# Performance work log

Hardware: AMD Instinct MI355X
Metric: run time of the kernel (lower is better)

The kernel has to match this reference:

```python
import jax, jax.numpy as jnp
import numpy as np


def mha_col0(x0, w_in, b_in, w_out, b_out):
    # x0: [N, D]. torch MHA (1 head, batch_first=False): seq dim = N, this is the
    # batch-0 slice (the only one consumed by tmp[:, 0]).
    qkv = x0 @ w_in.T + b_in                     # [N, 3D]
    q, k, v = jnp.split(qkv, 3, axis=-1)         # each [N, D]
    scale = 1.0 / np.sqrt(np.float32(q.shape[-1]))
    attn = jax.nn.softmax((q * scale) @ k.T, axis=-1)   # [N, N]
    return (attn @ v) @ w_out.T + b_out          # [N, D]


def sage(x_src, x_dst, ei, w_l, b_l, w_r):
    # PyG SAGEConv with aggr='sum': out = lin_l(sum_j x_src[src_j]) + lin_r(x_dst)
    msg = x_src[ei[0]]                                            # [E, D] gather
    agg = jax.ops.segment_sum(msg, ei[1], num_segments=x_dst.shape[0])  # [Nd, D] scatter
    return agg @ w_l.T + b_l + x_dst @ w_r.T


def setup_inputs() -> dict:
    key = jax.random.key(0)
    ks = jax.random.split(key, 24)
    N, C, D, E = 8192, 6, 128, 262144
    s = 0.05
    p = lambda k, shape: jax.random.normal(k, shape, dtype=jnp.float32) * s
    return {
        "x_A": jax.random.normal(ks[0], (N, C, D), dtype=jnp.float32),
        "x_B": jax.random.normal(ks[1], (N, C, D), dtype=jnp.float32),
        "ei_AB": jax.random.randint(ks[2], (2, E), 0, N),
        "ei_BA": jax.random.randint(ks[3], (2, E), 0, N),
        "ei_AA": jax.random.randint(ks[4], (2, E), 0, N),
        "inW_A": p(ks[5], (3 * D, D)), "inB_A": p(ks[6], (3 * D,)),
        "outW_A": p(ks[7], (D, D)), "outB_A": p(ks[8], (D,)),
        "inW_B": p(ks[9], (3 * D, D)), "inB_B": p(ks[10], (3 * D,)),
        "outW_B": p(ks[11], (D, D)), "outB_B": p(ks[12], (D,)),
        "wl_AB": p(ks[13], (D, D)), "bl_AB": p(ks[14], (D,)), "wr_AB": p(ks[15], (D, D)),
        "wl_BA": p(ks[16], (D, D)), "bl_BA": p(ks[17], (D,)), "wr_BA": p(ks[18], (D, D)),
        "wl_AA": p(ks[19], (D, D)), "bl_AA": p(ks[20], (D,)), "wr_AA": p(ks[21], (D, D)),
    }


def reference(x_A, x_B, ei_AB, ei_BA, ei_AA,
              inW_A, inB_A, outW_A, outB_A,
              inW_B, inB_B, outW_B, outB_B,
              wl_AB, bl_AB, wr_AB,
              wl_BA, bl_BA, wr_BA,
              wl_AA, bl_AA, wr_AA):
    # per-type attention, keeping only column 0 (tmp[:, 0])
    h_A = mha_col0(x_A[:, 0], inW_A, inB_A, outW_A, outB_A)   # [N, D]
    h_B = mha_col0(x_B[:, 0], inW_B, inB_B, outW_B, outB_B)   # [N, D]
    # HeteroConv(aggr='sum'): B gets A->B; A gets B->A + A->A
    out_B = sage(h_A, h_B, ei_AB, wl_AB, bl_AB, wr_AB)
    out_A = (sage(h_B, h_A, ei_BA, wl_BA, bl_BA, wr_BA)
             + sage(h_A, h_A, ei_AA, wl_AA, bl_AA, wr_AA))
    # re-attach remaining column tokens (x is 3D)
    new_A = jnp.concatenate((out_A[:, None, :], x_A[:, 1:]), axis=1)  # [N, C, D]
    new_B = jnp.concatenate((out_B[:, None, :], x_B[:, 1:]), axis=1)
    return new_A, new_B
```

## Files before the change

### kernel.cpp

```cpp
#include <hip/hip_runtime.h>
#include <hip/hip_bf16.h>

typedef unsigned short u16;
typedef unsigned int u32;
typedef __attribute__((ext_vector_type(8))) short bf16x8;
typedef __attribute__((ext_vector_type(4))) short bf16x4;
typedef __attribute__((ext_vector_type(4))) float f32x4;
typedef __attribute__((ext_vector_type(16))) float f32x16;

#define MFMA(a,b,c)   __builtin_amdgcn_mfma_f32_16x16x32_bf16((a),(b),(c),0,0,0)
#define MFMA32(a,b,c) __builtin_amdgcn_mfma_f32_32x32x16_bf16((a),(b),(c),0,0,0)

__device__ __forceinline__ float bf2f(u16 u){
  union { float f; u32 i; } c; c.i = ((u32)u) << 16; return c.f;
}
__device__ __forceinline__ u16 f2bf(float f){
  __hip_bfloat16 h = __float2bfloat16(f);
  u16 u; __builtin_memcpy(&u, &h, 2); return u;
}
__device__ __forceinline__ bf16x8 ld8f(const float* p){
  bf16x8 r;
  #pragma unroll
  for (int i = 0; i < 8; i++) r[i] = (short)f2bf(p[i]);
  return r;
}
__device__ __forceinline__ u32 cvtpk(float a, float b){
  u32 r; asm volatile("v_cvt_pk_bf16_f32 %0, %1, %2" : "=v"(r) : "v"(a), "v"(b)); return r;
}
__device__ __forceinline__ void pl32swap(u32 &a, u32 &b){
  asm volatile("v_permlane32_swap_b32 %0, %1" : "+v"(a), "+v"(b));
}

#define QSCALE 0.12751741528681559f

struct WPrepArgs { const float* src[10]; int off[10]; int total4; };
__global__ __launch_bounds__(256) void prelude_kernel(
    WPrepArgs a, u16* __restrict__ wdst,
    const int* __restrict__ e0, const int* __restrict__ e1, const int* __restrict__ e2,
    int* __restrict__ cnt,
    const float* __restrict__ xA, float* __restrict__ outA,
    const float* __restrict__ xB, float* __restrict__ outB,
    int Nn, int E, int W, int HB, int TB)
{
  const int tid = threadIdx.x;
  int b = blockIdx.x;
  if (b < W) {
    int i = b * 256 + tid;
    if (i >= a.total4) return;
    int e = i * 4;
    int j = 0;
    #pragma unroll
    for (int k = 1; k < 10; k++) if (e >= a.off[k]) j = k;
    f32x4 v = *(const f32x4*)(a.src[j] + (e - a.off[j]));
    bf16x4 o;
    #pragma unroll
    for (int r = 0; r < 4; r++) o[r] = (short)f2bf(v[r]);
    *(bf16x4*)(wdst + e) = o;
    return;
  }
  b -= W;
  if (b < 3 * HB) {
    int t = b / HB;
    int e = (b % HB) * 256 + tid;
    if (e >= E) return;
    const int* ei = t == 0 ? e0 : (t == 1 ? e1 : e2);
    atomicAdd(&cnt[t * Nn + ei[E + e]], 1);
    return;
  }
  b -= 3 * HB;
  {
    int t = b / TB;
    int idx = (b % TB) * 256 + tid;
    if (idx >= Nn * 160) return;
    const float* x = t ? xB : xA;
    float* o = t ? outB : outA;
    int n = idx / 160, r = idx % 160;
    size_t off = (size_t)n * 768 + 128 + (size_t)r * 4;
    *(f32x4*)(o + off) = *(const f32x4*)(x + off);
  }
}

__global__ __launch_bounds__(256) void qkv_scan_kernel(
    const float* __restrict__ xA, const u16* __restrict__ wA, const float* __restrict__ bA, u16* __restrict__ yA,
    const float* __restrict__ xB, const u16* __restrict__ wB, const float* __restrict__ bB, u16* __restrict__ yB,
    u16* __restrict__ vtA_, u16* __restrict__ vtB_,
    const int* __restrict__ cnt, int* __restrict__ off, int* __restrict__ work,
    int Nn, int N, int LB)
{
  const int tid = threadIdx.x;
  int b = blockIdx.x;
  if (b >= 2 * LB) {
    const int t = b - 2 * LB;
    const int* c = cnt + t * Nn;
    int* o = off + t * (Nn + 1);
    int* w = work + t * Nn;
    __shared__ int part[256];
    const int base = tid * 32;
    int loc[32], s = 0;
    #pragma unroll
    for (int i = 0; i < 32; i++) { loc[i] = s; s += c[base + i]; }
    part[tid] = s;
    __syncthreads();
    #pragma unroll
    for (int st = 1; st < 256; st <<= 1) {
      int v = (tid >= st) ? part[tid - st] : 0;
      __syncthreads();
      part[tid] += v;
      __syncthreads();
    }
    int pre = (tid == 0) ? 0 : part[tid - 1];
    #pragma unroll
    for (int i = 0; i < 32; i++) { int p = pre + loc[i]; o[base + i] = p; w[base + i] = p; }
    if (tid == 255) o[Nn] = part[255];
    return;
  }
  const int yb = b & 1, xb = b >> 1;
  const float* x = yb ? xB : xA;
  const u16* w = yb ? wB : wA;
  const float* bb = yb ? bB : bA;
  u16* y = yb ? yB : yA;
  u16* vt = yb ? vtB_ : vtA_;
  const int lane = tid & 63, wid = tid >> 6;
  const int g = lane >> 4, l15 = lane & 15;
  const int row0 = xb * 64 + wid * 16;

  bf16x8 a[4];
  const float* xr = x + (size_t)(row0 + l15) * 768;
  #pragma unroll
  for (int kk = 0; kk < 4; kk++) a[kk] = ld8f(xr + kk * 32 + g * 8);

  const f32x4 fz = {0.f, 0.f, 0.f, 0.f};
  for (int j0 = 0; j0 < 384; j0 += 16) {
    f32x4 acc = fz;
    const u16* wr_ = w + (size_t)(j0 + l15) * 128;
    #pragma unroll
    for (int kk = 0; kk < 4; kk++)
      acc = MFMA(a[kk], *(const bf16x8*)(wr_ + kk * 32 + g * 8), acc);
    float bv = bb[j0 + l15];
    if (j0 < 128) {
      #pragma unroll
      for (int r = 0; r < 4; r++)
        y[(size_t)(row0 + g * 4 + r) * 256 + j0 + l15] = f2bf((acc[r] + bv) * QSCALE);
    } else if (j0 < 256) {
      #pragma unroll
      for (int r = 0; r < 4; r++)
        y[(size_t)(row0 + g * 4 + r) * 256 + j0 + l15] = f2bf(acc[r] + bv);
    } else {
      bf16x4 o4;
      #pragma unroll
      for (int r = 0; r < 4; r++) o4[r] = (short)f2bf(acc[r] + bv);
      *(bf16x4*)(vt + (size_t)(j0 - 256 + l15) * N + row0 + g * 4) = o4;
    }
  }
}

__global__ __launch_bounds__(256, 2) void flash_sort_kernel(
    const u16* __restrict__ qkvA, const u16* __restrict__ vtA,
    const u16* __restrict__ qkvB, const u16* __restrict__ vtB,
    u16* __restrict__ part_acc, float* __restrict__ part_ml,
    const int* __restrict__ e0, const int* __restrict__ e1, const int* __restrict__ e2,
    int* __restrict__ work, int* __restrict__ ssrc,
    int N, int segsz, int SEG, int NB128, int FB, int HB, int E)
{
  __shared__ __align__(16) u16 Kt[2][64 * 128];
  __shared__ __align__(16) u16 Vtt[3][128 * 64];
  const int tid = threadIdx.x;
  int b = blockIdx.x;
  if (b >= FB) {
    int sb = b - FB;
    int t = sb / HB;
    int e = (sb % HB) * 256 + tid;
    if (e >= E) return;
    const int* ei = t == 0 ? e0 : (t == 1 ? e1 : e2);
    int s = ei[e], d = ei[E + e];
    int pos = atomicAdd(&work[t * N + d], 1);
    ssrc[(size_t)t * E + pos] = s;
    return;
  }
  const int x = b % NB128;
  const int rest = b / NB128;
  const int seg = rest % SEG;
  const int ty = rest / SEG;
  const u16* qkv = ty ? qkvB : qkvA;
  const u16* vt  = ty ? vtB  : vtA;
  const int lane = tid & 63, wid = tid >> 6;
  const int l31 = lane & 31, h = lane >> 5, l7 = lane & 7;
  const int q = x * 128 + wid * 32 + l31;
  const int kvbase = seg * segsz;
  const int nt = segsz >> 6;

  int rk[4], ck[4], cks[4], rv[4], cv[4], cvs[4];
  #pragma unroll
  for (int i = 0; i < 4; i++) {
    int ch = tid + i * 256;
    rk[i] = ch >> 4; ck[i] = (ch & 15) * 8; cks[i] = ck[i] ^ ((rk[i] & 7) << 3);
    rv[i] = ch >> 3; cv[i] = (ch & 7) * 8;  cvs[i] = cv[i] ^ ((rv[i] & 7) << 3);
  }

  bf16x8 aQ[8];
  const u16* qr = qkv + (size_t)q * 256;
  #pragma unroll
  for (int kk = 0; kk < 8; kk++) aQ[kk] = *(const bf16x8*)(qr + kk * 16 + h * 8);

  f32x16 accO[4];
  #pragma unroll
  for (int d = 0; d < 4; d++) accO[d] = (f32x16)0.f;
  float m_ = -INFINITY, l_ = 0.f;
  f32x16 scA[2], scB[2];
  bf16x8 kreg[4], vreg[4];

  #pragma unroll
  for (int i = 0; i < 4; i++) {
    kreg[i] = *(const bf16x8*)(qkv + 128 + (size_t)(kvbase + rk[i]) * 256 + ck[i]);
    vreg[i] = *(const bf16x8*)(vt + (size_t)rv[i] * N + kvbase + cv[i]);
  }
  #pragma unroll
  for (int i = 0; i < 4; i++) {
    *(bf16x8*)&Kt[0][rk[i] * 128 + cks[i]] = kreg[i];
    *(bf16x8*)&Vtt[0][rv[i] * 64 + cvs[i]] = vreg[i];
  }
  __syncthreads();
  if (nt > 1) {
    const int kv1 = kvbase + 64;
    #pragma unroll
    for (int i = 0; i < 4; i++) {
      kreg[i] = *(const bf16x8*)(qkv + 128 + (size_t)(kv1 + rk[i]) * 256 + ck[i]);
      vreg[i] = *(const bf16x8*)(vt + (size_t)rv[i] * N + kv1 + cv[i]);
    }
  }
  scA[0] = (f32x16)0.f; scA[1] = (f32x16)0.f;
  #pragma unroll
  for (int kk = 0; kk < 8; kk++) {
    const int co = ((kk * 2 + h) * 8) ^ (l7 << 3);
    bf16x8 aK0 = *(bf16x8*)&Kt[0][l31 * 128 + co];
    bf16x8 aK1 = *(bf16x8*)&Kt[0][(32 + l31) * 128 + co];
    scA[0] = MFMA32(aK0, aQ[kk], scA[0]);
    scA[1] = MFMA32(aK1, aQ[kk], scA[1]);
  }

  int t = 0, vb = 0;
  auto fstep = [&](f32x16* scIn, f32x16* scOut) {
    const bool hasN = (t + 1 < nt);
    const int kbN = (t + 1) & 1;
    const int vbN = (vb + 1 == 3) ? 0 : vb + 1;
    if (hasN) {
      #pragma unroll
      for (int i = 0; i < 4; i++) {
        *(bf16x8*)&Kt[kbN][rk[i] * 128 + cks[i]] = kreg[i];
        *(bf16x8*)&Vtt[vbN][rv[i] * 64 + cvs[i]] = vreg[i];
      }
    }
    __syncthreads();
    if (t + 2 < nt) {
      const int kv0n = kvbase + (t + 2) * 64;
      #pragma unroll
      for (int i = 0; i < 4; i++) {
        kreg[i] = *(const bf16x8*)(qkv + 128 + (size_t)(kv0n + rk[i]) * 256 + ck[i]);
        vreg[i] = *(const bf16x8*)(vt + (size_t)rv[i] * N + kv0n + cv[i]);
      }
    }
    if (hasN) {
      scOut[0] = (f32x16)0.f; scOut[1] = (f32x16)0.f;
      #pragma unroll
      for (int kk = 0; kk < 8; kk++) {
        const int co = ((kk * 2 + h) * 8) ^ (l7 << 3);
        bf16x8 aK0 = *(bf16x8*)&Kt[kbN][l31 * 128 + co];
        bf16x8 aK1 = *(bf16x8*)&Kt[kbN][(32 + l31) * 128 + co];
        scOut[0] = MFMA32(aK0, aQ[kk], scOut[0]);
        scOut[1] = MFMA32(aK1, aQ[kk], scOut[1]);
      }
    }
    float pmax = scIn[0][0];
    #pragma unroll
    for (int i = 1; i < 16; i++) pmax = fmaxf(pmax, scIn[0][i]);
    #pragma unroll
    for (int i = 0; i < 16; i++) pmax = fmaxf(pmax, scIn[1][i]);
    pmax = fmaxf(pmax, __shfl_xor(pmax, 32));
    if (!__all(pmax - m_ <= 8.0f)) {
      float nm = fmaxf(m_, pmax);
      float corr = __builtin_exp2f(m_ - nm);
      m_ = nm; l_ *= corr;
      #pragma unroll
      for (int d = 0; d < 4; d++)
        #pragma unroll
        for (int i = 0; i < 16; i++) accO[d][i] *= corr;
    }
    float sum = 0.f;
    #pragma unroll
    for (int i = 0; i < 16; i++) {
      float e0 = __builtin_exp2f(scIn[0][i] - m_);
      float e1 = __builtin_exp2f(scIn[1][i] - m_);
      scIn[0][i] = e0; scIn[1][i] = e1; sum += e0 + e1;
    }
    sum += __shfl_xor(sum, 32);
    l_ += sum;
    #pragma unroll
    for (int tt = 0; tt < 4; tt++) {
      const f32x16& s_ = scIn[tt >> 1];
      const int jA = (tt & 1) * 2, jB = jA + 1;
      u32 a0 = cvtpk(s_[jA * 4 + 0], s_[jA * 4 + 1]);
      u32 b0 = cvtpk(s_[jB * 4 + 0], s_[jB * 4 + 1]);
      u32 a1 = cvtpk(s_[jA * 4 + 2], s_[jA * 4 + 3]);
      u32 b1 = cvtpk(s_[jB * 4 + 2], s_[jB * 4 + 3]);
      pl32swap(a0, b0); pl32swap(a1, b1);
      union { u32 w[4]; bf16x8 v; } pf;
      pf.w[0] = a0; pf.w[1] = a1; pf.w[2] = b0; pf.w[3] = b1;
      #pragma unroll
      for (int db = 0; db < 4; db++) {
        bf16x8 aV = *(bf16x8*)&Vtt[vb][(db * 32 + l31) * 64 + (((tt * 2 + h) * 8) ^ (l7 << 3))];
        accO[db] = MFMA32(aV, pf.v, accO[db]);
      }
    }
    vb = vbN; ++t;
  };
  while (t < nt) { fstep(scA, scB); fstep(scB, scA); }

  const size_t pbase = ((size_t)(ty * SEG + seg) * N + q) * 128;
  #pragma unroll
  for (int d = 0; d < 4; d++)
    #pragma unroll
    for (int j = 0; j < 4; j++) {
      bf16x4 o4;
      #pragma unroll
      for (int r = 0; r < 4; r++) o4[r] = (short)f2bf(accO[d][j * 4 + r]);
      *(bf16x4*)(part_acc + pbase + d * 32 + j * 8 + h * 4) = o4;
    }
  if (h == 0) {
    float2 ml; ml.x = m_; ml.y = l_;
    *(float2*)(part_ml + ((size_t)(ty * SEG + seg) * N + q) * 2) = ml;
  }
}

__global__ __launch_bounds__(256) void combine_hproj_kernel(
    const u16* __restrict__ part_acc, const float* __restrict__ part_ml,
    const u16* __restrict__ woutA, const float* __restrict__ boutA, u16* __restrict__ hA,
    const u16* __restrict__ woutB, const float* __restrict__ boutB, u16* __restrict__ hB,
    int N, int SEG)
{
  __shared__ __align__(16) u16 ot[64 * 136];
  const int t = blockIdx.y;
  const u16* w = t ? woutB : woutA;
  const float* bb = t ? boutB : boutA;
  u16* hOut = t ? hB : hA;
  const int tid = threadIdx.x;
  const int row = tid >> 2, qt = tid & 3;
  const int grow = blockIdx.x * 64 + row;

  float m = -INFINITY;
  for (int s = 0; s < SEG; s++)
    m = fmaxf(m, part_ml[((size_t)(t * SEG + s) * N + grow) * 2]);
  float l = 0.f;
  float acc[32];
  #pragma unroll
  for (int i = 0; i < 32; i++) acc[i] = 0.f;
  for (int s = 0; s < SEG; s++) {
    const float* ml = part_ml + ((size_t)(t * SEG + s) * N + grow) * 2;
    float w8 = __builtin_exp2f(ml[0] - m);
    l += w8 * ml[1];
    const u16* pa = part_acc + ((size_t)(t * SEG + s) * N + grow) * 128 + qt * 32;
    #pragma unroll
    for (int j = 0; j < 4; j++) {
      bf16x8 vch = *(const bf16x8*)(pa + j * 8);
      #pragma unroll
      for (int i = 0; i < 8; i++) acc[j * 8 + i] += w8 * bf2f((u16)vch[i]);
    }
  }
  const float inv = 1.f / l;
  #pragma unroll
  for (int j = 0; j < 4; j++) {
    bf16x8 oc;
    #pragma unroll
    for (int i = 0; i < 8; i++) oc[i] = (short)f2bf(acc[j * 8 + i] * inv);
    *(bf16x8*)&ot[row * 136 + qt * 32 + j * 8] = oc;
  }
  __syncthreads();

  const int lane = tid & 63, wid = tid >> 6;
  const int g = lane >> 4, l15 = lane & 15;
  const int row0 = wid * 16;
  bf16x8 a[4];
  #pragma unroll
  for (int kk = 0; kk < 4; kk++) a[kk] = *(bf16x8*)&ot[(row0 + l15) * 136 + kk * 32 + g * 8];
  const f32x4 fz = {0.f, 0.f, 0.f, 0.f};
  for (int j0 = 0; j0 < 128; j0 += 16) {
    f32x4 acc2 = fz;
    const u16* wr_ = w + (size_t)(j0 + l15) * 128;
    #pragma unroll
    for (int kk = 0; kk < 4; kk++)
      acc2 = MFMA(a[kk], *(const bf16x8*)(wr_ + kk * 32 + g * 8), acc2);
    float bv = bb[j0 + l15];
    #pragma unroll
    for (int r = 0; r < 4; r++)
      hOut[(size_t)(blockIdx.x * 64 + row0 + g * 4 + r) * 128 + j0 + l15] = f2bf(acc2[r] + bv);
  }
}

__global__ __launch_bounds__(256) void aggregate_kernel(
    const u16* __restrict__ h0, const u16* __restrict__ h1, const u16* __restrict__ h2,
    const int* __restrict__ off, const int* __restrict__ ssrc,
    u16* __restrict__ agg, int Nn, int E)
{
  const int t = blockIdx.y;
  const u16* h = t == 0 ? h0 : (t == 1 ? h1 : h2);
  const int* o = off + t * (Nn + 1);
  const int* ss = ssrc + (size_t)t * E;
  u16* a = agg + (size_t)t * Nn * 128;
  const int wid = threadIdx.x >> 6, lane = threadIdx.x & 63;
  const int d = blockIdx.x * 4 + wid;
  const int s0 = o[d], s1 = o[d + 1];
  float a0 = 0.f, a1 = 0.f;
  int e = s0;
  for (; e + 3 < s1; e += 4) {
    int r0 = ss[e], r1 = ss[e + 1], r2 = ss[e + 2], r3 = ss[e + 3];
    u32 v0 = *(const u32*)(h + (size_t)r0 * 128 + lane * 2);
    u32 v1 = *(const u32*)(h + (size_t)r1 * 128 + lane * 2);
    u32 v2 = *(const u32*)(h + (size_t)r2 * 128 + lane * 2);
    u32 v3 = *(const u32*)(h + (size_t)r3 * 128 + lane * 2);
    a0 += bf2f((u16)(v0 & 0xffff)) + bf2f((u16)(v1 & 0xffff)) + bf2f((u16)(v2 & 0xffff)) + bf2f((u16)(v3 & 0xffff));
    a1 += bf2f((u16)(v0 >> 16)) + bf2f((u16)(v1 >> 16)) + bf2f((u16)(v2 >> 16)) + bf2f((u16)(v3 >> 16));
  }
  for (; e < s1; e++) {
    u32 v = *(const u32*)(h + (size_t)ss[e] * 128 + lane * 2);
    a0 += bf2f((u16)(v & 0xffff));
    a1 += bf2f((u16)(v >> 16));
  }
  *(u32*)(a + (size_t)d * 128 + lane * 2) = cvtpk(a0, a1);
}

__global__ __launch_bounds__(256) void sage_out_kernel(
    const u16* __restrict__ aggAB, const u16* __restrict__ wlAB, const float* __restrict__ blAB,
    const u16* __restrict__ hB, const u16* __restrict__ wrAB,
    const u16* __restrict__ aggBA, const u16* __restrict__ wlBA, const float* __restrict__ blBA,
    const u16* __restrict__ hA, const u16* __restrict__ wrBA,
    const u16* __restrict__ aggAA, const u16* __restrict__ wlAA, const float* __restrict__ blAA,
    const u16* __restrict__ wrAA,
    float* __restrict__ outA, float* __restrict__ outB)
{
  const bool two = (blockIdx.y == 1);
  const u16* agg1 = two ? aggBA : aggAB;
  const u16* wl1  = two ? wlBA  : wlAB;
  const float* bl1 = two ? blBA : blAB;
  const u16* h1   = two ? hA : hB;
  const u16* wr1  = two ? wrBA : wrAB;
  float* out = two ? outA : outB;

  const int lane = threadIdx.x & 63, wid = threadIdx.x >> 6;
  const int g = lane >> 4, l15 = lane & 15;
  const int row0 = blockIdx.x * 64 + wid * 16;

  bf16x8 a1[4], aH1[4], a2[4];
  const u16* ar1 = agg1 + (size_t)(row0 + l15) * 128;
  const u16* hr1 = h1 + (size_t)(row0 + l15) * 128;
  #pragma unroll
  for (int kk = 0; kk < 4; kk++) {
    a1[kk] = *(const bf16x8*)(ar1 + kk * 32 + g * 8);
    aH1[kk] = *(const bf16x8*)(hr1 + kk * 32 + g * 8);
  }
  if (two) {
    const u16* ar2 = aggAA + (size_t)(row0 + l15) * 128;
    #pragma unroll
    for (int kk = 0; kk < 4; kk++)
      a2[kk] = *(const bf16x8*)(ar2 + kk * 32 + g * 8);
  }

  const f32x4 fz = {0.f, 0.f, 0.f, 0.f};
  for (int j0 = 0; j0 < 128; j0 += 16) {
    f32x4 acc = fz;
    const u16* w1 = wl1 + (size_t)(j0 + l15) * 128;
    const u16* w2 = wr1 + (size_t)(j0 + l15) * 128;
    #pragma unroll
    for (int kk = 0; kk < 4; kk++) {
      acc = MFMA(a1[kk], *(const bf16x8*)(w1 + kk * 32 + g * 8), acc);
      acc = MFMA(aH1[kk], *(const bf16x8*)(w2 + kk * 32 + g * 8), acc);
    }
    float bias = bl1[j0 + l15];
    if (two) {
      const u16* w3 = wlAA + (size_t)(j0 + l15) * 128;
      const u16* w4 = wrAA + (size_t)(j0 + l15) * 128;
      #pragma unroll
      for (int kk = 0; kk < 4; kk++) {
        acc = MFMA(a2[kk], *(const bf16x8*)(w3 + kk * 32 + g * 8), acc);
        acc = MFMA(aH1[kk], *(const bf16x8*)(w4 + kk * 32 + g * 8), acc);
      }
      bias += blAA[j0 + l15];
    }
    #pragma unroll
    for (int r = 0; r < 4; r++)
      out[(size_t)(row0 + g * 4 + r) * 768 + j0 + l15] = acc[r] + bias;
  }
}

extern "C" void kernel_launch(void* const* d_in, const int* in_sizes, int n_in,
                              void* d_out, int out_size, void* d_ws, size_t ws_size,
                              hipStream_t stream)
{
  const int D = 128, C = 6;
  const int N = in_sizes[0] / (C * D);
  const int E = in_sizes[2] / 2;

  const float* xA = (const float*)d_in[0];
  const float* xB = (const float*)d_in[1];
  const int* eiAB = (const int*)d_in[2];
  const int* eiBA = (const int*)d_in[3];
  const int* eiAA = (const int*)d_in[4];
  const float* inW_A  = (const float*)d_in[5];
  const float* inB_A  = (const float*)d_in[6];
  const float* outW_A = (const float*)d_in[7];
  const float* outB_A = (const float*)d_in[8];
  const float* inW_B  = (const float*)d_in[9];
  const float* inB_B  = (const float*)d_in[10];
  const float* outW_B = (const float*)d_in[11];
  const float* outB_B = (const float*)d_in[12];
  const float* wlAB = (const float*)d_in[13];
  const float* blAB = (const float*)d_in[14];
  const float* wrAB = (const float*)d_in[15];
  const float* wlBA = (const float*)d_in[16];
  const float* blBA = (const float*)d_in[17];
  const float* wrBA = (const float*)d_in[18];
  const float* wlAA = (const float*)d_in[19];
  const float* blAA = (const float*)d_in[20];
  const float* wrAA = (const float*)d_in[21];

  u16* qkvA = (u16*)d_ws;
  u16* qkvB = qkvA + (size_t)N * 256;
  u16* vtA  = qkvB + (size_t)N * 256;
  u16* vtB  = vtA + (size_t)D * N;
  u16* hA   = vtB + (size_t)D * N;
  u16* hB   = hA + (size_t)N * D;
  u16* wbf  = hB + (size_t)N * D;
  const int wsz[10] = {3*D*D, 3*D*D, D*D, D*D, D*D, D*D, D*D, D*D, D*D, D*D};
  const float* wsrc[10] = {inW_A, inW_B, outW_A, outW_B, wlAB, wrAB, wlBA, wrBA, wlAA, wrAA};
  WPrepArgs wp; int wtot = 0;
  for (int k = 0; k < 10; k++) { wp.src[k] = wsrc[k]; wp.off[k] = wtot; wtot += wsz[k]; }
  wp.total4 = wtot / 4;
  u16* w_inA  = wbf + wp.off[0];
  u16* w_inB  = wbf + wp.off[1];
  u16* w_outA = wbf + wp.off[2];
  u16* w_outB = wbf + wp.off[3];
  u16* w_wlAB = wbf + wp.off[4];
  u16* w_wrAB = wbf + wp.off[5];
  u16* w_wlBA = wbf + wp.off[6];
  u16* w_wrBA = wbf + wp.off[7];
  u16* w_wlAA = wbf + wp.off[8];
  u16* w_wrAA = wbf + wp.off[9];

  int* cnt  = (int*)(wbf + wtot);
  int* off  = cnt + 3 * N;
  int* work = off + 3 * (N + 1);
  int* ssrc = work + 3 * N;
  char* uni = (char*)(ssrc + 3 * E);
  size_t base_b = (size_t)(uni - (char*)d_ws);
  size_t agg_b = (size_t)3 * N * 128 * 2;
  auto part_b = [&](int S){ return (size_t)2 * S * N * 128 * 2 + (size_t)2 * S * N * 2 * 4; };
  int SEG = 4;
  while (SEG > 1 && ws_size < base_b + (part_b(SEG) > agg_b ? part_b(SEG) : agg_b)) SEG >>= 1;
  const int segsz = N / SEG;
  u16* part_acc = (u16*)uni;
  float* part_ml = (float*)(part_acc + (size_t)2 * SEG * N * 128);
  u16* aggAB = (u16*)uni;
  u16* aggBA = aggAB + (size_t)N * D;
  u16* aggAA = aggBA + (size_t)N * D;

  float* outA = (float*)d_out;
  float* outB = outA + (size_t)N * C * D;

  dim3 blk(256);
  const int W = (wp.total4 + 255) / 256;
  const int HB = (E + 255) / 256;
  const int TB = (N * 160 + 255) / 256;
  const int LB = N / 64;
  const int NB128 = N / 128;
  const int FB = NB128 * SEG * 2;
  (void)hipMemsetAsync(cnt, 0, (size_t)3 * N * sizeof(int), stream);
  prelude_kernel<<<dim3(W + 3 * HB + 2 * TB), blk, 0, stream>>>(
      wp, wbf, eiAB, eiBA, eiAA, cnt, xA, outA, xB, outB, N, E, W, HB, TB);
  qkv_scan_kernel<<<dim3(2 * LB + 3), blk, 0, stream>>>(
      xA, w_inA, inB_A, qkvA, xB, w_inB, inB_B, qkvB, vtA, vtB,
      cnt, off, work, N, N, LB);
  flash_sort_kernel<<<dim3(FB + 3 * HB), blk, 0, stream>>>(
      qkvA, vtA, qkvB, vtB, part_acc, part_ml,
      eiAB, eiBA, eiAA, work, ssrc, N, segsz, SEG, NB128, FB, HB, E);
  combine_hproj_kernel<<<dim3(N / 64, 2), blk, 0, stream>>>(part_acc, part_ml,
                                                            w_outA, outB_A, hA,
                                                            w_outB, outB_B, hB, N, SEG);
  aggregate_kernel<<<dim3(N / 4, 3), blk, 0, stream>>>(hA, hB, hA, off, ssrc, aggAB, N, E);
  sage_out_kernel<<<dim3(N / 64, 2), blk, 0, stream>>>(
      aggAB, w_wlAB, blAB, hB, w_wrAB,
      aggBA, w_wlBA, blBA, hA, w_wrBA,
      aggAA, w_wlAA, blAA, w_wrAA, outA, outB);
}
```

Measured before the change: 236.1 us.

## Drop LDS staging in flash attention; read K/V directly from global memory

The flash attention kernel no longer stages K and V tiles through double/triple-buffered shared memory with barriers and register prefetch. Each wave now loads its MFMA operands for K and V straight from global memory (relying on L1/L2 caching). It also raises the launch-bounds occupancy hint to 3 blocks per CU and doubles the KV split count to 8 segments for more parallelism. The trade-off is redundant global/L2 traffic across the four waves and no explicit latency hiding, against removing LDS writes and syncs and gaining occupancy.

New measurement: 426.5 us. 1.81x slower.

```diff
diff --git a/kernel.cpp b/kernel.cpp
--- a/kernel.cpp
+++ b/kernel.cpp
@@ -154,7 +154,7 @@
   }
 }
 
-__global__ __launch_bounds__(256, 2) void flash_sort_kernel(
+__global__ __launch_bounds__(256, 3) void flash_sort_kernel(
     const u16* __restrict__ qkvA, const u16* __restrict__ vtA,
     const u16* __restrict__ qkvB, const u16* __restrict__ vtB,
     u16* __restrict__ part_acc, float* __restrict__ part_ml,
@@ -162,8 +162,6 @@
     int* __restrict__ work, int* __restrict__ ssrc,
     int N, int segsz, int SEG, int NB128, int FB, int HB, int E)
 {
-  __shared__ __align__(16) u16 Kt[2][64 * 128];
-  __shared__ __align__(16) u16 Vtt[3][128 * 64];
   const int tid = threadIdx.x;
   int b = blockIdx.x;
   if (b >= FB) {
@@ -184,18 +182,9 @@
   const u16* qkv = ty ? qkvB : qkvA;
   const u16* vt  = ty ? vtB  : vtA;
   const int lane = tid & 63, wid = tid >> 6;
-  const int l31 = lane & 31, h = lane >> 5, l7 = lane & 7;
+  const int l31 = lane & 31, h = lane >> 5;
   const int q = x * 128 + wid * 32 + l31;
   const int kvbase = seg * segsz;
-  const int nt = segsz >> 6;
-
-  int rk[4], ck[4], cks[4], rv[4], cv[4], cvs[4];
-  #pragma unroll
-  for (int i = 0; i < 4; i++) {
-    int ch = tid + i * 256;
-    rk[i] = ch >> 4; ck[i] = (ch & 15) * 8; cks[i] = ck[i] ^ ((rk[i] & 7) << 3);
-    rv[i] = ch >> 3; cv[i] = (ch & 7) * 8;  cvs[i] = cv[i] ^ ((rv[i] & 7) << 3);
-  }
 
   bf16x8 aQ[8];
   const u16* qr = qkv + (size_t)q * 256;
@@ -206,75 +195,27 @@
   #pragma unroll
   for (int d = 0; d < 4; d++) accO[d] = (f32x16)0.f;
   float m_ = -INFINITY, l_ = 0.f;
-  f32x16 scA[2], scB[2];
-  bf16x8 kreg[4], vreg[4];
-
-  #pragma unroll
-  for (int i = 0; i < 4; i++) {
-    kreg[i] = *(const bf16x8*)(qkv + 128 + (size_t)(kvbase + rk[i]) * 256 + ck[i]);
-    vreg[i] = *(const bf16x8*)(vt + (size_t)rv[i] * N + kvbase + cv[i]);
-  }
-  #pragma unroll
-  for (int i = 0; i < 4; i++) {
-    *(bf16x8*)&Kt[0][rk[i] * 128 + cks[i]] = kreg[i];
-    *(bf16x8*)&Vtt[0][rv[i] * 64 + cvs[i]] = vreg[i];
-  }
-  __syncthreads();
-  if (nt > 1) {
-    const int kv1 = kvbase + 64;
-    #pragma unroll
-    for (int i = 0; i < 4; i++) {
-      kreg[i] = *(const bf16x8*)(qkv + 128 + (size_t)(kv1 + rk[i]) * 256 + ck[i]);
-      vreg[i] = *(const bf16x8*)(vt + (size_t)rv[i] * N + kv1 + cv[i]);
-    }
-  }
-  scA[0] = (f32x16)0.f; scA[1] = (f32x16)0.f;
-  #pragma unroll
-  for (int kk = 0; kk < 8; kk++) {
-    const int co = ((kk * 2 + h) * 8) ^ (l7 << 3);
-    bf16x8 aK0 = *(bf16x8*)&Kt[0][l31 * 128 + co];
-    bf16x8 aK1 = *(bf16x8*)&Kt[0][(32 + l31) * 128 + co];
-    scA[0] = MFMA32(aK0, aQ[kk], scA[0]);
-    scA[1] = MFMA32(aK1, aQ[kk], scA[1]);
-  }
-
-  int t = 0, vb = 0;
-  auto fstep = [&](f32x16* scIn, f32x16* scOut) {
-    const bool hasN = (t + 1 < nt);
-    const int kbN = (t + 1) & 1;
-    const int vbN = (vb + 1 == 3) ? 0 : vb + 1;
-    if (hasN) {
-      #pragma unroll
-      for (int i = 0; i < 4; i++) {
-        *(bf16x8*)&Kt[kbN][rk[i] * 128 + cks[i]] = kreg[i];
-        *(bf16x8*)&Vtt[vbN][rv[i] * 64 + cvs[i]] = vreg[i];
-      }
-    }
-    __syncthreads();
-    if (t + 2 < nt) {
-      const int kv0n = kvbase + (t + 2) * 64;
-      #pragma unroll
-      for (int i = 0; i < 4; i++) {
-        kreg[i] = *(const bf16x8*)(qkv + 128 + (size_t)(kv0n + rk[i]) * 256 + ck[i]);
-        vreg[i] = *(const bf16x8*)(vt + (size_t)rv[i] * N + kv0n + cv[i]);
-      }
-    }
-    if (hasN) {
-      scOut[0] = (f32x16)0.f; scOut[1] = (f32x16)0.f;
-      #pragma unroll
-      for (int kk = 0; kk < 8; kk++) {
-        const int co = ((kk * 2 + h) * 8) ^ (l7 << 3);
-        bf16x8 aK0 = *(bf16x8*)&Kt[kbN][l31 * 128 + co];
-        bf16x8 aK1 = *(bf16x8*)&Kt[kbN][(32 + l31) * 128 + co];
-        scOut[0] = MFMA32(aK0, aQ[kk], scOut[0]);
-        scOut[1] = MFMA32(aK1, aQ[kk], scOut[1]);
-      }
-    }
-    float pmax = scIn[0][0];
-    #pragma unroll
-    for (int i = 1; i < 16; i++) pmax = fmaxf(pmax, scIn[0][i]);
-    #pragma unroll
-    for (int i = 0; i < 16; i++) pmax = fmaxf(pmax, scIn[1][i]);
+
+  const u16* kp = qkv + 128 + (size_t)l31 * 256 + h * 8;
+  const u16* vp = vt + (size_t)l31 * N + h * 8;
+
+  for (int kv0 = kvbase; kv0 < kvbase + segsz; kv0 += 64) {
+    const u16* kt0 = kp + (size_t)kv0 * 256;
+    const u16* kt1 = kt0 + 32 * 256;
+    f32x16 sc0 = (f32x16)0.f, sc1 = (f32x16)0.f;
+    #pragma unroll
+    for (int kk = 0; kk < 8; kk++) {
+      bf16x8 aK0 = *(const bf16x8*)(kt0 + kk * 16);
+      bf16x8 aK1 = *(const bf16x8*)(kt1 + kk * 16);
+      sc0 = MFMA32(aK0, aQ[kk], sc0);
+      sc1 = MFMA32(aK1, aQ[kk], sc1);
+    }
+
+    float pmax = sc0[0];
+    #pragma unroll
+    for (int i = 1; i < 16; i++) pmax = fmaxf(pmax, sc0[i]);
+    #pragma unroll
+    for (int i = 0; i < 16; i++) pmax = fmaxf(pmax, sc1[i]);
     pmax = fmaxf(pmax, __shfl_xor(pmax, 32));
     if (!__all(pmax - m_ <= 8.0f)) {
       float nm = fmaxf(m_, pmax);
@@ -288,15 +229,17 @@
     float sum = 0.f;
     #pragma unroll
     for (int i = 0; i < 16; i++) {
-      float e0 = __builtin_exp2f(scIn[0][i] - m_);
-      float e1 = __builtin_exp2f(scIn[1][i] - m_);
-      scIn[0][i] = e0; scIn[1][i] = e1; sum += e0 + e1;
+      float e0 = __builtin_exp2f(sc0[i] - m_);
+      float e1 = __builtin_exp2f(sc1[i] - m_);
+      sc0[i] = e0; sc1[i] = e1; sum += e0 + e1;
     }
     sum += __shfl_xor(sum, 32);
     l_ += sum;
+
+    const u16* vt0 = vp + kv0;
     #pragma unroll
     for (int tt = 0; tt < 4; tt++) {
-      const f32x16& s_ = scIn[tt >> 1];
+      const f32x16& s_ = (tt < 2) ? sc0 : sc1;
       const int jA = (tt & 1) * 2, jB = jA + 1;
       u32 a0 = cvtpk(s_[jA * 4 + 0], s_[jA * 4 + 1]);
       u32 b0 = cvtpk(s_[jB * 4 + 0], s_[jB * 4 + 1]);
@@ -307,13 +250,11 @@
       pf.w[0] = a0; pf.w[1] = a1; pf.w[2] = b0; pf.w[3] = b1;
       #pragma unroll
       for (int db = 0; db < 4; db++) {
-        bf16x8 aV = *(bf16x8*)&Vtt[vb][(db * 32 + l31) * 64 + (((tt * 2 + h) * 8) ^ (l7 << 3))];
+        bf16x8 aV = *(const bf16x8*)(vt0 + (size_t)(db * 32) * N + tt * 16);
         accO[db] = MFMA32(aV, pf.v, accO[db]);
       }
     }
-    vb = vbN; ++t;
-  };
-  while (t < nt) { fstep(scA, scB); fstep(scB, scA); }
+  }
 
   const size_t pbase = ((size_t)(ty * SEG + seg) * N + q) * 128;
   #pragma unroll
@@ -552,7 +493,7 @@
   size_t base_b = (size_t)(uni - (char*)d_ws);
   size_t agg_b = (size_t)3 * N * 128 * 2;
   auto part_b = [&](int S){ return (size_t)2 * S * N * 128 * 2 + (size_t)2 * S * N * 2 * 4; };
-  int SEG = 4;
+  int SEG = 8;
   while (SEG > 1 && ws_size < base_b + (part_b(SEG) > agg_b ? part_b(SEG) : agg_b)) SEG >>= 1;
   const int segsz = N / SEG;
   u16* part_acc = (u16*)uni;
```
